# Kernel tuning notes

Hardware: AMD Instinct MI355X
Metric: run time of the kernel (lower is better)

The kernel has to match this reference:

```python
import jax, jax.numpy as jnp
import numpy as np

B, T, S, C = 16, 2048, 512, 192
NEG = -1e9  # large-negative stand-in for float32.min (avoids overflow when accumulated)


def setup_inputs() -> dict:
    key = jax.random.key(0)
    ks = jax.random.split(key, 6)
    m_p = jax.random.normal(ks[0], (B, S, C), jnp.float32)
    logs_p = jax.random.normal(ks[1], (B, S, C), jnp.float32) * 0.1
    z_p = jax.random.normal(ks[2], (B, T, C), jnp.float32)
    logs_q = jax.random.normal(ks[3], (B, T, C), jnp.float32) * 0.1
    textlen = jax.random.randint(ks[4], (B,), S // 2, S + 1, jnp.int32)
    mellen = jax.random.randint(ks[5], (B,), T // 2, T + 1, jnp.int32)
    return dict(m_p=m_p, logs_p=logs_p, z_p=z_p, logs_q=logs_q,
                textlen=textlen, mellen=mellen)


def monotonic_alignment_search(ll, textlen, mellen):
    """Viterbi-style monotonic alignment. ll: [B, T, S] -> attn [B, T, S]."""
    Bb, Tt, Ss = ll.shape
    s_range = jnp.arange(Ss)
    ll_t = jnp.transpose(ll, (1, 0, 2))  # [T, B, S]

    def fwd(prob, xt):
        t, ll_row = xt
        prev = jnp.concatenate([jnp.full((Bb, 1), NEG, ll.dtype), prob[:, :-1]], axis=1)
        stay = prob >= prev  # True: best path stays at same text index
        prob = jnp.where(s_range[None] <= t, jnp.maximum(prob, prev) + ll_row, NEG)
        return prob, stay

    _, direction = jax.lax.scan(fwd, jnp.zeros((Bb, Ss), ll.dtype),
                                (jnp.arange(Tt), ll_t))  # direction: [T, B, S] bool

    def bwd(idx, xt):
        t, dir_t = xt
        active = t < mellen  # [B]
        onehot = (s_range[None] == idx[:, None]) & active[:, None]  # [B, S]
        stay = jnp.take_along_axis(dir_t, idx[:, None], axis=1)[:, 0]
        new_idx = jnp.where(active, idx - (1 - stay.astype(jnp.int32)), idx)
        return new_idx, onehot

    _, attn_rev = jax.lax.scan(bwd, textlen - 1,
                               (jnp.arange(Tt - 1, -1, -1), direction[::-1]))
    attn = attn_rev[::-1].astype(ll.dtype)  # [T, B, S]
    return jnp.transpose(attn, (1, 0, 2))


def reference(m_p, logs_p, z_p, logs_q, textlen, mellen):
    tmask = (jnp.arange(S)[None] < textlen[:, None]).astype(jnp.float32)  # [B, S]
    mmask = (jnp.arange(T)[None] < mellen[:, None]).astype(jnp.float32)   # [B, T]
    attnmask = mmask[:, :, None] * tmask[:, None]                          # [B, T, S]

    # Negative cross-entropy score matrix [B, T, S]
    s_sq_r = jnp.exp(-2.0 * logs_p)  # [B, S, C]
    nc1 = jnp.sum(-0.5 * np.log(2.0 * np.pi) - logs_p, axis=-1)[:, None]  # [B, 1, S]
    nc2 = jnp.einsum('btc,bsc->bts', -0.5 * z_p ** 2, s_sq_r)
    nc3 = jnp.einsum('btc,bsc->bts', z_p, m_p * s_sq_r)
    nc4 = jnp.sum(-0.5 * m_p ** 2 * s_sq_r, axis=-1)[:, None]             # [B, 1, S]
    neg_cent = nc1 + nc2 + nc3 + nc4

    ll = jnp.where(attnmask > 0, neg_cent, NEG)
    attn = jax.lax.stop_gradient(monotonic_alignment_search(ll, textlen, mellen))

    # Expand text-level stats to frame level via the hard alignment
    m_e = jnp.einsum('bts,bsc->btc', attn, m_p)
    l_e = jnp.einsum('bts,bsc->btc', attn, logs_p)

    kl = l_e - logs_q - 0.5 + 0.5 * (z_p - m_e) ** 2 * jnp.exp(-2.0 * l_e)
    kl = jnp.sum(kl * mmask[..., None]) / jnp.sum(mmask)
    return kl, attn
```

## Files before the change

kernel.cpp:

```cpp
#include <hip/hip_runtime.h>

#define NEGV (-1e9f)

static const int B_ = 16;
static const int T_ = 2048;
static const int S_ = 512;
static const int C_ = 192;

typedef unsigned short ushort_t;
using f32x4 = __attribute__((ext_vector_type(4))) float;
using s16x8 = __attribute__((ext_vector_type(8))) short;

__device__ __forceinline__ void split2(float x, ushort_t& h, ushort_t& l) {
    __bf16 hb = (__bf16)x;
    h = __builtin_bit_cast(ushort_t, hb);
    float r = x - (float)hb;
    __bf16 lb = (__bf16)r;
    l = __builtin_bit_cast(ushort_t, lb);
}

__device__ __forceinline__ ushort_t to_bf16(float x) {
    return __builtin_bit_cast(ushort_t, (__bf16)x);
}

__global__ __launch_bounds__(256)
void prep_kernel(const float* __restrict__ m_p, const float* __restrict__ logs_p,
                 ushort_t* __restrict__ Bh, ushort_t* __restrict__ Bl,
                 float* __restrict__ nc14) {
    int wid = (blockIdx.x * blockDim.x + threadIdx.x) >> 6;
    int lane = threadIdx.x & 63;
    if (wid >= B_ * S_) return;
    const float HALF_LOG_2PI = 0.9189385332046727f;
    const float* mrow = m_p    + (size_t)wid * C_;
    const float* lrow = logs_p + (size_t)wid * C_;
    ushort_t* bh = Bh + (size_t)wid * 384;
    ushort_t* bl = Bl + (size_t)wid * 384;
    float tot = 0.f;
#pragma unroll
    for (int q = 0; q < 3; ++q) {
        int c = lane + q * 64;
        float m  = mrow[c];
        float lp = lrow[c];
        float s2r = __expf(-2.f * lp);
        float a = m * s2r;
        ushort_t h, l;
        split2(a, h, l);   bh[c] = h;        bl[c] = l;
        split2(s2r, h, l); bh[192 + c] = h;  bl[192 + c] = l;
        tot += (-HALF_LOG_2PI - lp) + (-0.5f * m * m * s2r);
    }
#pragma unroll
    for (int off = 32; off > 0; off >>= 1) tot += __shfl_xor(tot, off);
    if (lane == 0) nc14[wid] = tot;
}

#define LDP 40
__global__ __launch_bounds__(256)
void gemm_kernel(const float* __restrict__ z_p,
                 const ushort_t* __restrict__ Bh, const ushort_t* __restrict__ Bl,
                 const float* __restrict__ nc14,
                 const int* __restrict__ textlen, const int* __restrict__ mellen,
                 float* __restrict__ ll) {
    __shared__ ushort_t sAh[128 * LDP];
    __shared__ ushort_t sBh[128 * LDP];
    __shared__ ushort_t sBl[128 * LDP];

    const int b  = blockIdx.z;
    const int t0 = blockIdx.y * 128;
    const int s0 = blockIdx.x * 128;
    const int tid = threadIdx.x;
    const int lane = tid & 63;
    const int wave = tid >> 6;
    const int wr = wave >> 1, wc = wave & 1;
    const int srow = tid >> 1;
    const int cb = (tid & 1) * 16;

    const int ml = mellen[b], tl = textlen[b];
    const int r15 = lane & 15;
    const int klane = (lane >> 4) * 8;

    if (t0 >= ml || s0 >= tl) {
        int scol[4];
#pragma unroll
        for (int n = 0; n < 4; ++n) scol[n] = s0 + wc * 64 + n * 16 + r15;
#pragma unroll
        for (int m = 0; m < 4; ++m) {
            const int tb = t0 + wr * 64 + m * 16 + (lane >> 4) * 4;
#pragma unroll
            for (int r = 0; r < 4; ++r) {
                float* orow = ll + ((size_t)b * T_ + tb + r) * S_;
#pragma unroll
                for (int n = 0; n < 4; ++n) orow[scol[n]] = NEGV;
            }
        }
        return;
    }

    f32x4 acc[4][4];
#pragma unroll
    for (int m = 0; m < 4; ++m)
#pragma unroll
        for (int n = 0; n < 4; ++n) acc[m][n] = (f32x4){0.f, 0.f, 0.f, 0.f};

    for (int kk = 0; kk < 12; ++kk) {
        {
            const int ck = (kk < 6 ? kk * 32 : (kk - 6) * 32) + cb;
            const float* src = z_p + ((size_t)b * T_ + t0 + srow) * C_ + ck;
            float e[16];
            *(float4*)(e + 0)  = *(const float4*)(src + 0);
            *(float4*)(e + 4)  = *(const float4*)(src + 4);
            *(float4*)(e + 8)  = *(const float4*)(src + 8);
            *(float4*)(e + 12) = *(const float4*)(src + 12);
            if (kk >= 6) {
#pragma unroll
                for (int i = 0; i < 16; ++i) e[i] = -0.5f * e[i] * e[i];
            }
            ushort_t h[16];
#pragma unroll
            for (int i = 0; i < 16; ++i) h[i] = to_bf16(e[i]);
            ushort_t* dh = &sAh[srow * LDP + cb];
            *(uint4*)dh = make_uint4(h[0] | (h[1] << 16), h[2] | (h[3] << 16),
                                     h[4] | (h[5] << 16), h[6] | (h[7] << 16));
            *(uint4*)(dh + 8) = make_uint4(h[8] | (h[9] << 16), h[10] | (h[11] << 16),
                                           h[12] | (h[13] << 16), h[14] | (h[15] << 16));
        }
        {
            const size_t off = ((size_t)b * S_ + s0 + srow) * 384 + kk * 32 + cb;
            const uint4 u0 = *(const uint4*)(Bh + off);
            const uint4 u1 = *(const uint4*)(Bh + off + 8);
            const uint4 v0 = *(const uint4*)(Bl + off);
            const uint4 v1 = *(const uint4*)(Bl + off + 8);
            ushort_t* dh = &sBh[srow * LDP + cb];
            ushort_t* dl = &sBl[srow * LDP + cb];
            *(uint4*)dh = u0; *(uint4*)(dh + 8) = u1;
            *(uint4*)dl = v0; *(uint4*)(dl + 8) = v1;
        }
        __syncthreads();

        s16x8 ah[4], bhf[4], blf[4];
#pragma unroll
        for (int m = 0; m < 4; ++m) {
            const int row = wr * 64 + m * 16 + r15;
            ah[m] = *(const s16x8*)&sAh[row * LDP + klane];
        }
#pragma unroll
        for (int n = 0; n < 4; ++n) {
            const int row = wc * 64 + n * 16 + r15;
            bhf[n] = *(const s16x8*)&sBh[row * LDP + klane];
            blf[n] = *(const s16x8*)&sBl[row * LDP + klane];
        }
#pragma unroll
        for (int m = 0; m < 4; ++m)
#pragma unroll
            for (int n = 0; n < 4; ++n) {
                acc[m][n] = __builtin_amdgcn_mfma_f32_16x16x32_bf16(ah[m], bhf[n], acc[m][n], 0, 0, 0);
                acc[m][n] = __builtin_amdgcn_mfma_f32_16x16x32_bf16(ah[m], blf[n], acc[m][n], 0, 0, 0);
            }
        __syncthreads();
    }

    int scol[4]; float ncv[4];
#pragma unroll
    for (int n = 0; n < 4; ++n) {
        scol[n] = s0 + wc * 64 + n * 16 + r15;
        ncv[n] = nc14[b * S_ + scol[n]];
    }
#pragma unroll
    for (int m = 0; m < 4; ++m) {
        const int tb = t0 + wr * 64 + m * 16 + (lane >> 4) * 4;
#pragma unroll
        for (int r = 0; r < 4; ++r) {
            const int t = tb + r;
            const bool tm = (t < ml);
            float* orow = ll + ((size_t)b * T_ + t) * S_;
#pragma unroll
            for (int n = 0; n < 4; ++n)
                orow[scol[n]] = (tm && scol[n] < tl) ? (acc[m][n][r] + ncv[n]) : NEGV;
        }
    }
}

__global__ __launch_bounds__(64)
void mas_forward(const float* __restrict__ ll, unsigned char* __restrict__ dir) {
    const int b = blockIdx.x;
    const int lane = threadIdx.x;
    const float* llb = ll + (size_t)b * T_ * S_ + lane * 8;
    unsigned char* db = dir + ((size_t)b * T_) * 64 + lane;
    const int sbase = lane * 8;

    float4 pre[8][2];
#pragma unroll
    for (int r = 0; r < 8; ++r) {
        pre[r][0] = *(const float4*)(llb + (size_t)r * S_);
        pre[r][1] = *(const float4*)(llb + (size_t)r * S_ + 4);
    }

    float p[8];
#pragma unroll
    for (int j = 0; j < 8; ++j) p[j] = 0.f;
    float carry = (lane == 0) ? NEGV : 0.f;

    auto step = [&](int t, int ph, bool masked) {
        float cur[8];
        cur[0] = pre[ph][0].x; cur[1] = pre[ph][0].y;
        cur[2] = pre[ph][0].z; cur[3] = pre[ph][0].w;
        cur[4] = pre[ph][1].x; cur[5] = pre[ph][1].y;
        cur[6] = pre[ph][1].z; cur[7] = pre[ph][1].w;
        const int tn = t + 8;
        if (tn < T_) {
            pre[ph][0] = *(const float4*)(llb + (size_t)tn * S_);
            pre[ph][1] = *(const float4*)(llb + (size_t)tn * S_ + 4);
        }
        float v7 = fmaxf(p[7], p[6]) + cur[7];
        float nc7 = masked ? ((sbase + 7 <= t) ? v7 : NEGV) : v7;
        float newcarry = __shfl_up(nc7, 1);

        unsigned bits = (p[0] >= carry) ? 1u : 0u;
#pragma unroll
        for (int j = 1; j < 8; ++j)
            bits |= (p[j] >= p[j - 1] ? 1u : 0u) << j;

        float nv[8];
        nv[0] = fmaxf(p[0], carry) + cur[0];
#pragma unroll
        for (int j = 1; j < 7; ++j) nv[j] = fmaxf(p[j], p[j - 1]) + cur[j];
        nv[7] = v7;
        if (masked) {
#pragma unroll
            for (int j = 0; j < 8; ++j)
                p[j] = (sbase + j <= t) ? nv[j] : NEGV;
        } else {
#pragma unroll
            for (int j = 0; j < 8; ++j) p[j] = nv[j];
        }
        carry = (lane == 0) ? NEGV : newcarry;
        db[(size_t)t * 64] = (unsigned char)bits;
    };

    for (int to = 0; to < S_ / 8; ++to) {
#pragma unroll
        for (int ph = 0; ph < 8; ++ph) step(to * 8 + ph, ph, true);
    }
    for (int to = S_ / 8; to < T_ / 8; ++to) {
#pragma unroll
        for (int ph = 0; ph < 8; ++ph) step(to * 8 + ph, ph, false);
    }
}

__global__ __launch_bounds__(64)
void mas_backward(const unsigned char* __restrict__ dir,
                  const int* __restrict__ textlen, const int* __restrict__ mellen,
                  int* __restrict__ idx_arr) {
    const int b = blockIdx.x;
    const int lane = threadIdx.x;
    const int tl = textlen[b], ml = mellen[b];
    for (int t = ml + lane; t < T_; t += 64) idx_arr[b * T_ + t] = -1;
    const unsigned char* db = dir + (size_t)b * T_ * 64;
    int idx = tl - 1;
    int t_hi = ml - 1;
    while (t_hi >= 0) {
        const int lo = idx - 7;
        const int blo = (lo > 0 ? lo : 0) >> 3;
        const int bhi = idx >> 3;
        const int t = t_hi - lane;
        unsigned v = 0;
        if (lane < 8 && t >= 0) {
            unsigned b0 = db[(size_t)t * 64 + blo];
            unsigned b1 = db[(size_t)t * 64 + bhi];
            v = b0 | (b1 << 8);
        }
        unsigned vk[8];
#pragma unroll
        for (int k = 0; k < 8; ++k) vk[k] = __shfl((int)v, k);
        int emit = -1;
#pragma unroll
        for (int k = 0; k < 8; ++k) {
            const int tt = t_hi - k;
            if (tt < 0) break;
            if (lane == k) emit = idx;
            const int sb = idx >> 3;
            const unsigned byte = (sb == bhi) ? (vk[k] >> 8) : (vk[k] & 0xffu);
            const int stay = (byte >> (idx & 7)) & 1;
            idx -= (1 - stay);
            if (idx < 0) idx = 0;
        }
        const int tt = t_hi - lane;
        if (lane < 8 && tt >= 0) idx_arr[b * T_ + tt] = emit;
        t_hi -= 8;
    }
}

__global__ __launch_bounds__(256)
void attn_kl(const float* __restrict__ m_p, const float* __restrict__ logs_p,
             const float* __restrict__ z_p, const float* __restrict__ logs_q,
             const int* __restrict__ idx_arr, const int* __restrict__ mellen,
             float* __restrict__ attn, float* __restrict__ frame_kl) {
    const int wid = (blockIdx.x * blockDim.x + threadIdx.x) >> 6;
    const int lane = threadIdx.x & 63;
    if (wid >= B_ * T_) return;
    const int b = wid >> 11;
    const int t = wid & (T_ - 1);
    const int ml = mellen[b];
    const int idx = idx_arr[wid];

    float* row = attn + (size_t)wid * S_;
#pragma unroll
    for (int j = 0; j < 8; ++j) {
        const int s = j * 64 + lane;
        row[s] = (s == idx) ? 1.0f : 0.0f;
    }

    float total = 0.f;
    if (t < ml) {
        const float* mr = m_p    + ((size_t)b * S_ + idx) * C_;
        const float* lr = logs_p + ((size_t)b * S_ + idx) * C_;
        const float* zr = z_p    + (size_t)wid * C_;
        const float* qr = logs_q + (size_t)wid * C_;
#pragma unroll
        for (int q = 0; q < 3; ++q) {
            const int c = lane + q * 64;
            const float le = lr[c];
            const float d = zr[c] - mr[c];
            total += le - qr[c] - 0.5f + 0.5f * d * d * __expf(-2.f * le);
        }
    }
#pragma unroll
    for (int off = 32; off > 0; off >>= 1) total += __shfl_xor(total, off);
    if (lane == 0) frame_kl[wid] = total;
}

__global__ __launch_bounds__(256)
void kl_reduce(const float* __restrict__ frame_kl, const int* __restrict__ mellen,
               float* __restrict__ out) {
    __shared__ float sm[256];
    const int tid = threadIdx.x;
    float s = 0.f;
    for (int k = tid; k < B_ * T_; k += 256) s += frame_kl[k];
    sm[tid] = s;
    __syncthreads();
    for (int off = 128; off > 0; off >>= 1) {
        if (tid < off) sm[tid] += sm[tid + off];
        __syncthreads();
    }
    if (tid == 0) {
        int sum_ml = 0;
        for (int bq = 0; bq < B_; ++bq) sum_ml += mellen[bq];
        out[0] = sm[0] / (float)sum_ml;
    }
}

extern "C" void kernel_launch(void* const* d_in, const int* in_sizes, int n_in,
                              void* d_out, int out_size, void* d_ws, size_t ws_size,
                              hipStream_t stream) {
    const float* m_p    = (const float*)d_in[0];
    const float* logs_p = (const float*)d_in[1];
    const float* z_p    = (const float*)d_in[2];
    const float* logs_q = (const float*)d_in[3];
    const int*   textlen = (const int*)d_in[4];
    const int*   mellen  = (const int*)d_in[5];

    float* out = (float*)d_out;
    float* attn = out + 1;
    float* ll = attn;

    char* ws = (char*)d_ws;
    const size_t OFF_BH   = 0;
    const size_t OFF_BL   = OFF_BH + (size_t)B_ * S_ * 384 * 2;
    const size_t OFF_NC   = OFF_BL + (size_t)B_ * S_ * 384 * 2;
    const size_t OFF_DIR  = OFF_NC + (size_t)B_ * S_ * 4;
    const size_t OFF_IDX  = OFF_DIR + (size_t)B_ * T_ * 64;
    const size_t OFF_FKL  = OFF_IDX + (size_t)B_ * T_ * 4;
    ushort_t* Bh = (ushort_t*)(ws + OFF_BH);
    ushort_t* Bl = (ushort_t*)(ws + OFF_BL);
    float* nc14 = (float*)(ws + OFF_NC);
    unsigned char* dir = (unsigned char*)(ws + OFF_DIR);
    int* idx_arr = (int*)(ws + OFF_IDX);
    float* frame_kl = (float*)(ws + OFF_FKL);

    prep_kernel<<<(B_ * S_) / 4, 256, 0, stream>>>(m_p, logs_p, Bh, Bl, nc14);
    gemm_kernel<<<dim3(S_ / 128, T_ / 128, B_), 256, 0, stream>>>(
        z_p, Bh, Bl, nc14, textlen, mellen, ll);
    mas_forward<<<B_, 64, 0, stream>>>(ll, dir);
    mas_backward<<<B_, 64, 0, stream>>>(dir, textlen, mellen, idx_arr);
    attn_kl<<<(B_ * T_) / 4, 256, 0, stream>>>(m_p, logs_p, z_p, logs_q,
                                               idx_arr, mellen, attn, frame_kl);
    kl_reduce<<<1, 256, 0, stream>>>(frame_kl, mellen, out);
}
```

Measured before the change: 486.7 us.

## Prefetch direction-bit windows two steps ahead in MAS backward

```diff
diff --git a/kernel.cpp b/kernel.cpp
--- a/kernel.cpp
+++ b/kernel.cpp
@@ -257,34 +257,48 @@
     const unsigned char* db = dir + (size_t)b * T_ * 64;
     int idx = tl - 1;
     int t_hi = ml - 1;
+
+    auto loadwin = [&](int throw_, int anchor, int& base) -> unsigned {
+        const int B = anchor >> 3;
+        const int b0 = (B > 3) ? (B - 3) : 0;
+        base = b0;
+        unsigned w = 0;
+        const int t = throw_ - lane;
+        if (lane < 8 && t >= 0) {
+            const unsigned char* p = db + (size_t)t * 64 + b0;
+            w = (unsigned)p[0] | ((unsigned)p[1] << 8) |
+                ((unsigned)p[2] << 16) | ((unsigned)p[3] << 24);
+        }
+        return w;
+    };
+
+    int b00, b01;
+    unsigned w0 = loadwin(t_hi, idx, b00);
+    unsigned w1 = loadwin(t_hi - 8, idx, b01);
+
     while (t_hi >= 0) {
-        const int lo = idx - 7;
-        const int blo = (lo > 0 ? lo : 0) >> 3;
-        const int bhi = idx >> 3;
-        const int t = t_hi - lane;
-        unsigned v = 0;
-        if (lane < 8 && t >= 0) {
-            unsigned b0 = db[(size_t)t * 64 + blo];
-            unsigned b1 = db[(size_t)t * 64 + bhi];
-            v = b0 | (b1 << 8);
-        }
+        int b02;
+        unsigned w2 = loadwin(t_hi - 16, idx, b02);
+
         unsigned vk[8];
 #pragma unroll
-        for (int k = 0; k < 8; ++k) vk[k] = __shfl((int)v, k);
+        for (int k = 0; k < 8; ++k) vk[k] = __shfl((int)w0, k);
         int emit = -1;
 #pragma unroll
         for (int k = 0; k < 8; ++k) {
             const int tt = t_hi - k;
             if (tt < 0) break;
             if (lane == k) emit = idx;
-            const int sb = idx >> 3;
-            const unsigned byte = (sb == bhi) ? (vk[k] >> 8) : (vk[k] & 0xffu);
+            const int off = (idx >> 3) - b00;
+            const unsigned byte = (vk[k] >> (off * 8)) & 0xffu;
             const int stay = (byte >> (idx & 7)) & 1;
             idx -= (1 - stay);
             if (idx < 0) idx = 0;
         }
         const int tt = t_hi - lane;
         if (lane < 8 && tt >= 0) idx_arr[b * T_ + tt] = emit;
+        w0 = w1; b00 = b01;
+        w1 = w2; b01 = b02;
         t_hi -= 8;
     }
 }
```

Measured after the change: 485.4 us, median of 2. About the same (-0.3%).
